# Kernel tuning notes

Hardware: AMD Instinct MI355X
Metric: run time of the kernel (lower is better)

## Reference

```python
import jax, jax.numpy as jnp
import numpy as np

N = 500_000      # total nodes in batched graph
B = 2_048        # number of graphs (segments)
D = 256          # input_dim == hidden_dim == output_dim


def setup_inputs() -> dict:
    key = jax.random.key(0)
    k = jax.random.split(key, 8)
    feat = jax.random.normal(k[0], (N, D), dtype=jnp.float32)
    cnt = jax.random.uniform(k[1], (N,), dtype=jnp.float32)
    segment_ids = jnp.sort(jax.random.randint(k[2], (N,), 0, B, dtype=jnp.int32))
    last_nodes = jax.random.randint(k[3], (B,), 0, N, dtype=jnp.int32)
    # learned parameters (torch nn.Linear: y = x @ W.T + b)
    s = 1.0 / np.sqrt(D)
    W_u = jax.random.uniform(k[4], (D, D), dtype=jnp.float32, minval=-s, maxval=s)
    W_v = jax.random.uniform(k[5], (D, D), dtype=jnp.float32, minval=-s, maxval=s)
    b_v = jax.random.uniform(k[6], (D,), dtype=jnp.float32, minval=-s, maxval=s)
    w_e = jax.random.uniform(k[7], (D,), dtype=jnp.float32, minval=-s, maxval=s)
    return {"feat": feat, "cnt": cnt, "segment_ids": segment_ids,
            "last_nodes": last_nodes, "W_u": W_u, "W_v": W_v,
            "b_v": b_v, "w_e": w_e}


def reference(feat, cnt, segment_ids, last_nodes, W_u, W_v, b_v, w_e):
    # fc_u: per-node projection  [N, D]
    feat_u = feat @ W_u.T
    # fc_v on last node of each graph, then broadcast back to nodes
    feat_v = feat[last_nodes] @ W_v.T + b_v          # [B, D]
    feat_vb = feat_v[segment_ids]                    # [N, D] broadcast_nodes
    # fc_e(sigmoid(u + v)) -> scalar gate per node
    e = jax.nn.sigmoid(feat_u + feat_vb) @ w_e       # [N]
    alpha = e * cnt                                  # [N]
    # segment-sum readout over graphs
    rst = jax.ops.segment_sum(feat * alpha[:, None], segment_ids,
                              num_segments=B)        # [B, D]
    return rst
```

## Files before the change

### kernel.cpp

```cpp
#include <hip/hip_runtime.h>
#include <hip/hip_bf16.h>

typedef __attribute__((ext_vector_type(8))) short short8;
typedef __attribute__((ext_vector_type(4))) float f32x4;

#define D 256
#define MT 64
#define NW 8
#define GRID_MAIN 256
#define G 8

__device__ __forceinline__ unsigned short f2bf(float f) {
    unsigned int u = __float_as_uint(f);
    u += 0x7FFFu + ((u >> 16) & 1u);
    return (unsigned short)(u >> 16);
}
__device__ __forceinline__ unsigned pack2(float a, float b) {
    return (unsigned)f2bf(a) | ((unsigned)f2bf(b) << 16);
}
__device__ __forceinline__ float bf2f(unsigned short s) {
    return __uint_as_float(((unsigned int)s) << 16);
}
__device__ __forceinline__ float fast_sigmoid(float x) {
    return __builtin_amdgcn_rcpf(1.f + __expf(-x));
}

__global__ void k_convert(const float* __restrict__ W, unsigned short* __restrict__ Wb, int n) {
    int i = blockIdx.x * 256 + threadIdx.x;
    if (i < n) Wb[i] = f2bf(W[i]);
}

__global__ __launch_bounds__(256) void k_featv(
    const float* __restrict__ feat, const int* __restrict__ last_nodes,
    const float* __restrict__ Wv, const float* __restrict__ bv,
    float* __restrict__ featv, int Bseg) {
    __shared__ float fln[G][D];
    const int t  = threadIdx.x;
    const int b0 = blockIdx.x * G;
    for (int g = 0; g < G; ++g) {
        int b = b0 + g;
        int ln = (b < Bseg) ? last_nodes[b] : 0;
        fln[g][t] = feat[(long)ln * D + t];
    }
    __syncthreads();
    float acc[G];
    float bvj = bv[t];
    #pragma unroll
    for (int g = 0; g < G; ++g) acc[g] = bvj;
    const float* wr = Wv + (long)t * D;
    for (int k = 0; k < D; k += 4) {
        float4 w4 = *(const float4*)(wr + k);
        #pragma unroll
        for (int g = 0; g < G; ++g) {
            acc[g] += w4.x * fln[g][k]     + w4.y * fln[g][k + 1]
                    + w4.z * fln[g][k + 2] + w4.w * fln[g][k + 3];
        }
    }
    for (int g = 0; g < G; ++g)
        if (b0 + g < Bseg) featv[(long)(b0 + g) * D + t] = acc[g];
}

__global__ __launch_bounds__(512, 2) void k_main(
    const float* __restrict__ feat, const float* __restrict__ cnt,
    const int* __restrict__ seg, const unsigned short* __restrict__ Wub,
    const float* __restrict__ featv, const float* __restrict__ we,
    float* __restrict__ rst, int N) {

    __shared__ unsigned short Abuf[2][MT][D];
    __shared__ float e_s[NW][MT];
    __shared__ int   seg_s[2][MT];
    __shared__ float cnt_s[2][MT];
    __shared__ float alpha_s[MT];

    const int t  = threadIdx.x;
    const int w  = t >> 6;
    const int l  = t & 63;
    const int rl = l & 15;
    const int h  = l >> 4;

    const int T   = (N + MT - 1) / MT;
    const int nb  = gridDim.x;
    const int per = T / nb, rem = T % nb;
    const int bid = blockIdx.x;
    const int c0  = bid * per + (bid < rem ? bid : rem);
    const int c1  = c0 + per + (bid < rem ? 1 : 0);
    if (c0 >= c1) return;

    short8 a_reg[2][8];
    {
        const unsigned short* ab = Wub + (long)(32 * w + rl) * D + h * 8;
        #pragma unroll
        for (int mt = 0; mt < 2; ++mt)
            #pragma unroll
            for (int s = 0; s < 8; ++s)
                a_reg[mt][s] = *(const short8*)(ab + (long)mt * 16 * D + s * 32);
    }
    f32x4 wev[2];
    wev[0] = *(const f32x4*)(we + 32 * w + h * 4);
    wev[1] = *(const f32x4*)(we + 32 * w + 16 + h * 4);

    {
        const long m0 = (long)c0 * MT;
        float4 sv[8];
        #pragma unroll
        for (int k = 0; k < 8; ++k) {
            long n = m0 + w * 8 + k; if (n > (long)N - 1) n = (long)N - 1;
            sv[k] = *(const float4*)(feat + n * D + 4 * l);
        }
        int sr = 0; float cr = 0.f;
        if (t < MT) {
            long n = m0 + t;
            if (n < N) { sr = seg[n]; cr = cnt[n]; }
            else       { sr = seg[N - 1]; cr = 0.f; }
        }
        #pragma unroll
        for (int k = 0; k < 8; ++k) {
            int R = w * 8 + k;
            uint2 v = make_uint2(pack2(sv[k].x, sv[k].y), pack2(sv[k].z, sv[k].w));
            *(uint2*)&Abuf[0][R][(((l >> 1) ^ k) << 3) + (l & 1) * 4] = v;
        }
        if (t < MT) { seg_s[0][t] = sr; cnt_s[0][t] = cr; }
        __syncthreads();
    }

    int cur = 0;
    for (int tt = c0; tt < c1; ++tt, cur ^= 1) {
        const int n0  = tt * MT;
        const int nv  = min(MT, N - n0);
        const bool more = (tt + 1 < c1);
        const int* seg_t = seg_s[cur];

        int sgv[4];
        #pragma unroll
        for (int nt = 0; nt < 4; ++nt) sgv[nt] = seg_t[nt * 16 + rl];

        f32x4 fvr[2][4];
        #pragma unroll
        for (int nt = 0; nt < 4; ++nt) {
            const float* fb = featv + (long)sgv[nt] * D + 32 * w + h * 4;
            fvr[0][nt] = *(const f32x4*)(fb);
            fvr[1][nt] = *(const f32x4*)(fb + 16);
        }
        asm volatile("" ::: "memory");

        float4 sv[8];
        int sr = 0; float cr = 0.f;
        if (more) {
            const long m1 = (long)(tt + 1) * MT;
            #pragma unroll
            for (int k = 0; k < 8; ++k) {
                long n = m1 + w * 8 + k; if (n > (long)N - 1) n = (long)N - 1;
                sv[k] = *(const float4*)(feat + n * D + 4 * l);
            }
            if (t < MT) {
                long n = m1 + t;
                if (n < N) { sr = seg[n]; cr = cnt[n]; }
                else       { sr = seg[N - 1]; cr = 0.f; }
            }
        }
        asm volatile("" ::: "memory");

        f32x4 acc[2][4];
        #pragma unroll
        for (int mt = 0; mt < 2; ++mt)
            #pragma unroll
            for (int nt = 0; nt < 4; ++nt) acc[mt][nt] = (f32x4)0.f;

        const unsigned short* Ab = &Abuf[cur][0][0];
        #pragma unroll
        for (int s = 0; s < 8; ++s) {
            short8 bfr[4];
            #pragma unroll
            for (int nt = 0; nt < 4; ++nt) {
                int R = nt * 16 + rl;
                int gr = (s * 4 + h) ^ (rl & 7);
                bfr[nt] = *(const short8*)(Ab + R * D + gr * 8);
            }
            #pragma unroll
            for (int mt = 0; mt < 2; ++mt)
                #pragma unroll
                for (int nt = 0; nt < 4; ++nt)
                    acc[mt][nt] = __builtin_amdgcn_mfma_f32_16x16x32_bf16(a_reg[mt][s], bfr[nt], acc[mt][nt], 0, 0, 0);
        }

        float ep[4] = {0.f, 0.f, 0.f, 0.f};
        #pragma unroll
        for (int mt = 0; mt < 2; ++mt)
            #pragma unroll
            for (int nt = 0; nt < 4; ++nt)
                #pragma unroll
                for (int r = 0; r < 4; ++r)
                    ep[nt] += wev[mt][r] * fast_sigmoid(acc[mt][nt][r] + fvr[mt][nt][r]);
        #pragma unroll
        for (int nt = 0; nt < 4; ++nt) {
            ep[nt] += __shfl_xor(ep[nt], 16);
            ep[nt] += __shfl_xor(ep[nt], 32);
        }
        if (h == 0) {
            #pragma unroll
            for (int nt = 0; nt < 4; ++nt) e_s[w][nt * 16 + rl] = ep[nt];
        }
        asm volatile("s_waitcnt lgkmcnt(0)\ns_barrier" ::: "memory");

        if (t < MT) {
            float e = 0.f;
            #pragma unroll
            for (int q = 0; q < NW; ++q) e += e_s[q][t];
            alpha_s[t] = e * cnt_s[cur][t];
        }
        asm volatile("s_waitcnt lgkmcnt(0)\ns_barrier" ::: "memory");

        if (more) {
            #pragma unroll
            for (int k = 0; k < 8; ++k) {
                int R = w * 8 + k;
                uint2 v = make_uint2(pack2(sv[k].x, sv[k].y), pack2(sv[k].z, sv[k].w));
                *(uint2*)&Abuf[cur ^ 1][R][(((l >> 1) ^ k) << 3) + (l & 1) * 4] = v;
            }
            if (t < MT) { seg_s[cur ^ 1][t] = sr; cnt_s[cur ^ 1][t] = cr; }
        }

        {
            const int halfq = t >> 8;
            const int d     = t & 255;
            const int i0    = halfq * 32;
            const int i1v   = min(i0 + 32, nv);
            const int dg = d >> 3, db = d & 7;
            if (i0 < i1v) {
                if ((i1v - i0) == 32 && seg_t[i0] == seg_t[i1v - 1]) {
                    float c0a = 0.f, c1a = 0.f, c2a = 0.f, c3a = 0.f;
                    #pragma unroll
                    for (int i2 = 0; i2 < 32; i2 += 4) {
                        int i = i0 + i2;
                        c0a += bf2f(Ab[(i + 0) * D + (((dg ^ ((i + 0) & 7))) << 3) + db]) * alpha_s[i + 0];
                        c1a += bf2f(Ab[(i + 1) * D + (((dg ^ ((i + 1) & 7))) << 3) + db]) * alpha_s[i + 1];
                        c2a += bf2f(Ab[(i + 2) * D + (((dg ^ ((i + 2) & 7))) << 3) + db]) * alpha_s[i + 2];
                        c3a += bf2f(Ab[(i + 3) * D + (((dg ^ ((i + 3) & 7))) << 3) + db]) * alpha_s[i + 3];
                    }
                    atomicAdd(&rst[(long)seg_t[i0] * D + d], (c0a + c1a) + (c2a + c3a));
                } else {
                    float c = 0.f;
                    int curseg = seg_t[i0];
                    for (int i = i0; i < i1v; ++i) {
                        int sgi = seg_t[i];
                        if (sgi != curseg) { atomicAdd(&rst[(long)curseg * D + d], c); c = 0.f; curseg = sgi; }
                        c += bf2f(Ab[i * D + ((dg ^ (i & 7)) << 3) + db]) * alpha_s[i];
                    }
                    atomicAdd(&rst[(long)curseg * D + d], c);
                }
            }
        }
        asm volatile("s_waitcnt lgkmcnt(0)\ns_barrier" ::: "memory");
    }
}

extern "C" void kernel_launch(void* const* d_in, const int* in_sizes, int n_in,
                              void* d_out, int out_size, void* d_ws, size_t ws_size,
                              hipStream_t stream) {
    const float* feat = (const float*)d_in[0];
    const float* cnt  = (const float*)d_in[1];
    const int*   segp = (const int*)d_in[2];
    const int*   last = (const int*)d_in[3];
    const float* Wu   = (const float*)d_in[4];
    const float* Wv   = (const float*)d_in[5];
    const float* bv   = (const float*)d_in[6];
    const float* we   = (const float*)d_in[7];
    float* rst = (float*)d_out;

    const int N    = in_sizes[1];
    const int Bseg = in_sizes[3];

    unsigned short* Wub   = (unsigned short*)d_ws;
    float*          featv = (float*)((char*)d_ws + (size_t)D * D * sizeof(unsigned short));

    hipMemsetAsync(d_out, 0, (size_t)out_size * sizeof(float), stream);
    k_convert<<<(D * D + 255) / 256, 256, 0, stream>>>(Wu, Wub, D * D);
    k_featv<<<(Bseg + G - 1) / G, 256, 0, stream>>>(feat, last, Wv, bv, featv, Bseg);
    k_main<<<GRID_MAIN, 512, 0, stream>>>(feat, cnt, segp, Wub, featv, we, rst, N);
}
```

Measured before the change: 199.0 us.

## Retune grid and occupancy, add MFMA priority, vectorize segment-sum reads

Doubles the main grid and the featv batch size, and raises launch bounds to 4 blocks per CU. Wraps the MFMA loop in s_setprio, swaps the hand-written bf16 conversion for the HIP intrinsic, and restructures the segment-sum so each thread reads packed bf16 pairs as 32-bit words over 16 rows instead of 32. The aim is more latency hiding and fewer LDS instructions. In exchange it risks register spills under the tighter launch bound and doubles the number of atomic adds.

```diff
diff --git a/kernel.cpp b/kernel.cpp
--- a/kernel.cpp
+++ b/kernel.cpp
@@ -7,19 +7,12 @@
 #define D 256
 #define MT 64
 #define NW 8
-#define GRID_MAIN 256
-#define G 8
-
-__device__ __forceinline__ unsigned short f2bf(float f) {
-    unsigned int u = __float_as_uint(f);
-    u += 0x7FFFu + ((u >> 16) & 1u);
-    return (unsigned short)(u >> 16);
-}
+#define GRID_MAIN 512
+#define G 16
+
 __device__ __forceinline__ unsigned pack2(float a, float b) {
-    return (unsigned)f2bf(a) | ((unsigned)f2bf(b) << 16);
-}
-__device__ __forceinline__ float bf2f(unsigned short s) {
-    return __uint_as_float(((unsigned int)s) << 16);
+    __hip_bfloat162 h = __float22bfloat162_rn(make_float2(a, b));
+    return *(unsigned*)&h;
 }
 __device__ __forceinline__ float fast_sigmoid(float x) {
     return __builtin_amdgcn_rcpf(1.f + __expf(-x));
@@ -27,7 +20,7 @@
 
 __global__ void k_convert(const float* __restrict__ W, unsigned short* __restrict__ Wb, int n) {
     int i = blockIdx.x * 256 + threadIdx.x;
-    if (i < n) Wb[i] = f2bf(W[i]);
+    if (i < n) Wb[i] = (unsigned short)(pack2(W[i], 0.f) & 0xffffu);
 }
 
 __global__ __launch_bounds__(256) void k_featv(
@@ -60,7 +53,7 @@
         if (b0 + g < Bseg) featv[(long)(b0 + g) * D + t] = acc[g];
 }
 
-__global__ __launch_bounds__(512, 2) void k_main(
+__global__ __launch_bounds__(512, 4) void k_main(
     const float* __restrict__ feat, const float* __restrict__ cnt,
     const int* __restrict__ seg, const unsigned short* __restrict__ Wub,
     const float* __restrict__ featv, const float* __restrict__ we,
@@ -167,6 +160,7 @@
             for (int nt = 0; nt < 4; ++nt) acc[mt][nt] = (f32x4)0.f;
 
         const unsigned short* Ab = &Abuf[cur][0][0];
+        __builtin_amdgcn_s_setprio(1);
         #pragma unroll
         for (int s = 0; s < 8; ++s) {
             short8 bfr[4];
@@ -182,6 +176,7 @@
                 for (int nt = 0; nt < 4; ++nt)
                     acc[mt][nt] = __builtin_amdgcn_mfma_f32_16x16x32_bf16(a_reg[mt][s], bfr[nt], acc[mt][nt], 0, 0, 0);
         }
+        __builtin_amdgcn_s_setprio(0);
 
         float ep[4] = {0.f, 0.f, 0.f, 0.f};
         #pragma unroll
@@ -221,32 +216,45 @@
         }
 
         {
-            const int halfq = t >> 8;
-            const int d     = t & 255;
-            const int i0    = halfq * 32;
-            const int i1v   = min(i0 + 32, nv);
-            const int dg = d >> 3, db = d & 7;
+            const int p   = t & 127;
+            const int gq  = t >> 7;
+            const int i0  = gq * 16;
+            const int i1v = min(i0 + 16, nv);
+            const unsigned* Ab32 = (const unsigned*)Ab;
             if (i0 < i1v) {
-                if ((i1v - i0) == 32 && seg_t[i0] == seg_t[i1v - 1]) {
-                    float c0a = 0.f, c1a = 0.f, c2a = 0.f, c3a = 0.f;
+                if ((i1v - i0) == 16 && seg_t[i0] == seg_t[i1v - 1]) {
+                    float ca = 0.f, cb = 0.f, ca2 = 0.f, cb2 = 0.f;
                     #pragma unroll
-                    for (int i2 = 0; i2 < 32; i2 += 4) {
+                    for (int i2 = 0; i2 < 16; i2 += 2) {
                         int i = i0 + i2;
-                        c0a += bf2f(Ab[(i + 0) * D + (((dg ^ ((i + 0) & 7))) << 3) + db]) * alpha_s[i + 0];
-                        c1a += bf2f(Ab[(i + 1) * D + (((dg ^ ((i + 1) & 7))) << 3) + db]) * alpha_s[i + 1];
-                        c2a += bf2f(Ab[(i + 2) * D + (((dg ^ ((i + 2) & 7))) << 3) + db]) * alpha_s[i + 2];
-                        c3a += bf2f(Ab[(i + 3) * D + (((dg ^ ((i + 3) & 7))) << 3) + db]) * alpha_s[i + 3];
+                        unsigned v0 = Ab32[(i + 0) * 128 + (((p >> 2) ^ ((i + 0) & 7)) << 2) + (p & 3)];
+                        unsigned v1 = Ab32[(i + 1) * 128 + (((p >> 2) ^ ((i + 1) & 7)) << 2) + (p & 3)];
+                        float a0 = alpha_s[i + 0], a1 = alpha_s[i + 1];
+                        ca  += __uint_as_float(v0 << 16) * a0;
+                        cb  += __uint_as_float(v0 & 0xffff0000u) * a0;
+                        ca2 += __uint_as_float(v1 << 16) * a1;
+                        cb2 += __uint_as_float(v1 & 0xffff0000u) * a1;
                     }
-                    atomicAdd(&rst[(long)seg_t[i0] * D + d], (c0a + c1a) + (c2a + c3a));
+                    long rb = (long)seg_t[i0] * D + 2 * p;
+                    atomicAdd(&rst[rb],     ca + ca2);
+                    atomicAdd(&rst[rb + 1], cb + cb2);
                 } else {
-                    float c = 0.f;
+                    float ca = 0.f, cb = 0.f;
                     int curseg = seg_t[i0];
                     for (int i = i0; i < i1v; ++i) {
                         int sgi = seg_t[i];
-                        if (sgi != curseg) { atomicAdd(&rst[(long)curseg * D + d], c); c = 0.f; curseg = sgi; }
-                        c += bf2f(Ab[i * D + ((dg ^ (i & 7)) << 3) + db]) * alpha_s[i];
+                        if (sgi != curseg) {
+                            long rb = (long)curseg * D + 2 * p;
+                            atomicAdd(&rst[rb], ca); atomicAdd(&rst[rb + 1], cb);
+                            ca = cb = 0.f; curseg = sgi;
+                        }
+                        unsigned v = Ab32[i * 128 + (((p >> 2) ^ (i & 7)) << 2) + (p & 3)];
+                        float al = alpha_s[i];
+                        ca += __uint_as_float(v << 16) * al;
+                        cb += __uint_as_float(v & 0xffff0000u) * al;
                     }
-                    atomicAdd(&rst[(long)curseg * D + d], c);
+                    long rb = (long)curseg * D + 2 * p;
+                    atomicAdd(&rst[rb], ca); atomicAdd(&rst[rb + 1], cb);
                 }
             }
         }
```

Result: slower. 478.4 us (+140.4%).
